# Optimization experiments

Hardware: AMD Instinct MI355X
Metric: run time of the kernel (lower is better)

The kernel has to match this reference:

```python
import jax, jax.numpy as jnp
import numpy as np

N, P, D = 262144, 128, 64
EPS = 1e-5
NEG = -1e30


def setup_inputs() -> dict:
    key = jax.random.key(0)
    ks = jax.random.split(key, 12)
    feature = jax.random.normal(ks[0], (N, D), jnp.float32)
    feature_geo = jax.random.normal(ks[1], (N, D), jnp.float32)
    xyz = jax.random.uniform(ks[2], (N, 3), jnp.float32)
    centers = jax.random.uniform(ks[3], (3,), jnp.float32)
    plane_center = jax.random.uniform(ks[4], (P, 3), jnp.float32)
    nrm = jax.random.normal(ks[5], (P, 3), jnp.float32)
    plane_normal = nrm / jnp.linalg.norm(nrm, axis=1, keepdims=True)
    lo = 0.3 * jax.random.uniform(ks[6], (P, 3), jnp.float32)
    hi = 0.5 + 0.5 * jax.random.uniform(ks[7], (P, 3), jnp.float32)
    # exactly two active axes per plane (one axis of the aabb is zeroed)
    ax = jnp.arange(P) % 3
    keep = (jnp.arange(3)[None, :] != ax[:, None]).astype(jnp.float32)
    plane_xyz_min = lo * keep
    plane_xyz_max = hi * keep
    w1 = 0.05 * jax.random.normal(ks[8], (2 * D, D), jnp.float32)
    b1 = jnp.zeros((D,), jnp.float32)
    w2 = 0.05 * jax.random.normal(ks[9], (D, D), jnp.float32)
    b2 = jnp.zeros((D,), jnp.float32)
    w3 = 0.05 * jax.random.normal(ks[10], (D, 1), jnp.float32)
    b3 = jnp.zeros((1,), jnp.float32)
    g1 = jnp.ones((D,), jnp.float32); be1 = jnp.zeros((D,), jnp.float32)
    m1 = jnp.zeros((D,), jnp.float32); v1 = jnp.ones((D,), jnp.float32)
    g2 = jnp.ones((D,), jnp.float32); be2 = jnp.zeros((D,), jnp.float32)
    m2 = jnp.zeros((D,), jnp.float32); v2 = jnp.ones((D,), jnp.float32)
    return dict(feature=feature, feature_geo=feature_geo, xyz=xyz, centers=centers,
                plane_center=plane_center, plane_normal=plane_normal,
                plane_xyz_min=plane_xyz_min, plane_xyz_max=plane_xyz_max,
                w1=w1, b1=b1, g1=g1, be1=be1, m1=m1, v1=v1,
                w2=w2, b2=b2, g2=g2, be2=be2, m2=m2, v2=v2,
                w3=w3, b3=b3)


def _bn(x, g, b, m, v):
    return (x - m) * (g * jax.lax.rsqrt(v + EPS)) + b


def reference(feature, feature_geo, xyz, centers, plane_center, plane_normal,
              plane_xyz_min, plane_xyz_max, w1, b1, g1, be1, m1, v1,
              w2, b2, g2, be2, m2, v2, w3, b3):
    clouds = xyz + centers                                   # [N,3]
    f = jnp.concatenate([feature, feature_geo], axis=1)      # [N,2D]
    # 1x1 conv MLP == per-point matmul (fc1 -> fc2 with BN+ReLU, fc3)
    h1 = jax.nn.relu(_bn(f @ w1 + b1, g1, be1, m1, v1))      # [N,D]
    h2 = jax.nn.relu(_bn(h1 @ w2 + b2, g2, be2, m2, v2))     # [N,D]
    scores = jax.nn.relu(h2 @ w3 + b3)[:, 0]                 # [N]
    # per-plane aabb mask over the two active axes (xyz_max != 0)
    active = plane_xyz_max != 0                              # [P,3]
    in_rng = (clouds[None] >= plane_xyz_min[:, None]) & (clouds[None] < plane_xyz_max[:, None])
    range_mask = jnp.all(in_rng | ~active[:, None, :], axis=-1)   # [P,N]
    # point-to-plane distance: |(clouds - center) . normal|
    dots = clouds @ plane_normal.T                           # [N,P]
    offs = jnp.sum(plane_center * plane_normal, axis=1)      # [P]
    dist = jnp.abs(dots - offs[None, :]).T                   # [P,N]
    mask = range_mask & (dist < 0.1)                         # [P,N]
    sig = jax.nn.sigmoid(scores)                             # [N]
    on_mask = mask & (sig > 0.5)[None, :]
    off_mask = mask & (sig <= 0.5)[None, :]

    def pool(m):  # masked max-pool of fc2 features over points of one plane
        val = jnp.max(jnp.where(m[:, None], h2, NEG), axis=0)     # [D]
        return jnp.where(jnp.any(m), val, 0.0)

    on_feat = jax.lax.map(pool, on_mask)                     # [P,D]
    off_feat = jax.lax.map(pool, off_mask)                   # [P,D]
    scores_masked = jnp.where(mask, scores[None, :], 0.0)    # [P,N]
    return scores_masked, mask, on_mask, off_mask, on_feat, off_feat
```

## Files before the change

kernel.cpp:

```cpp
#include <hip/hip_runtime.h>
#include <hip/hip_bf16.h>
#include <math.h>

#define NPTS 262144
#define NP   128
#define DD   64
#define NWORDS (NPTS / 64)

__global__ __launch_bounds__(256) void prep_kernel(
    const float* __restrict__ plane_center, const float* __restrict__ plane_normal,
    const float* __restrict__ pmin, const float* __restrict__ pmax,
    float* __restrict__ packed, float* __restrict__ out_feats)
{
    const int t = threadIdx.x;
    out_feats[blockIdx.x * 256 + t] = 0.0f;
    if (blockIdx.x == 0 && t < NP) {
        float n0 = plane_normal[t*3+0], n1 = plane_normal[t*3+1], n2 = plane_normal[t*3+2];
        float c0 = plane_center[t*3+0], c1 = plane_center[t*3+1], c2 = plane_center[t*3+2];
        float off = (c0*n0 + c1*n1) + c2*n2;
        float4* pp = reinterpret_cast<float4*>(packed) + t * 3;
        pp[0] = make_float4(n0, n1, n2, off);
        pp[1] = make_float4(pmin[t*3+0], pmin[t*3+1], pmin[t*3+2], 0.0f);
        pp[2] = make_float4(pmax[t*3+0], pmax[t*3+1], pmax[t*3+2], 0.0f);
    }
}

__global__ __launch_bounds__(256) void fused_kernel(
    const float* __restrict__ feature, const float* __restrict__ feature_geo,
    const float* __restrict__ xyz, const float* __restrict__ centers,
    const float* __restrict__ packed,
    const float* __restrict__ w1, const float* __restrict__ b1,
    const float* __restrict__ g1, const float* __restrict__ be1,
    const float* __restrict__ m1, const float* __restrict__ v1,
    const float* __restrict__ w2, const float* __restrict__ b2,
    const float* __restrict__ g2, const float* __restrict__ be2,
    const float* __restrict__ m2, const float* __restrict__ v2,
    const float* __restrict__ w3, const float* __restrict__ b3,
    float* __restrict__ h2_out,
    float* __restrict__ out_sm, float* __restrict__ out_mask,
    float* __restrict__ out_on, float* __restrict__ out_off,
    unsigned long long* __restrict__ hitOn, unsigned long long* __restrict__ hitOff)
{
    const int t = threadIdx.x;
    const int n = blockIdx.x * 256 + t;

    const float c0 = xyz[n*3+0] + centers[0];
    const float c1 = xyz[n*3+1] + centers[1];
    const float c2 = xyz[n*3+2] + centers[2];

    float acc[DD];
#pragma unroll
    for (int j = 0; j < DD; ++j) acc[j] = 0.0f;

    const float4* fA = reinterpret_cast<const float4*>(feature) + (size_t)n * 16;
#pragma unroll 1
    for (int q = 0; q < 16; ++q) {
        const float4 fv = fA[q];
        const float* wr = w1 + q * 4 * DD;
#pragma unroll
        for (int j = 0; j < DD; ++j) acc[j] = fmaf(fv.x, wr[j], acc[j]);
#pragma unroll
        for (int j = 0; j < DD; ++j) acc[j] = fmaf(fv.y, wr[DD + j], acc[j]);
#pragma unroll
        for (int j = 0; j < DD; ++j) acc[j] = fmaf(fv.z, wr[2 * DD + j], acc[j]);
#pragma unroll
        for (int j = 0; j < DD; ++j) acc[j] = fmaf(fv.w, wr[3 * DD + j], acc[j]);
    }
    const float4* fB = reinterpret_cast<const float4*>(feature_geo) + (size_t)n * 16;
    const float* w1b = w1 + DD * DD;
#pragma unroll 1
    for (int q = 0; q < 16; ++q) {
        const float4 fv = fB[q];
        const float* wr = w1b + q * 4 * DD;
#pragma unroll
        for (int j = 0; j < DD; ++j) acc[j] = fmaf(fv.x, wr[j], acc[j]);
#pragma unroll
        for (int j = 0; j < DD; ++j) acc[j] = fmaf(fv.y, wr[DD + j], acc[j]);
#pragma unroll
        for (int j = 0; j < DD; ++j) acc[j] = fmaf(fv.z, wr[2 * DD + j], acc[j]);
#pragma unroll
        for (int j = 0; j < DD; ++j) acc[j] = fmaf(fv.w, wr[3 * DD + j], acc[j]);
    }
    float h1[DD];
#pragma unroll
    for (int j = 0; j < DD; ++j) {
        float sc = g1[j] * (1.0f / sqrtf(v1[j] + 1e-5f));
        float h  = fmaf(acc[j] + b1[j] - m1[j], sc, be1[j]);
        h1[j] = fmaxf(h, 0.0f);
        acc[j] = 0.0f;
    }
#pragma unroll 1
    for (int q = 0; q < 16; ++q) {
        const float fx = h1[4*q+0], fy = h1[4*q+1], fz = h1[4*q+2], fw = h1[4*q+3];
        const float* wr = w2 + q * 4 * DD;
#pragma unroll
        for (int j = 0; j < DD; ++j) acc[j] = fmaf(fx, wr[j], acc[j]);
#pragma unroll
        for (int j = 0; j < DD; ++j) acc[j] = fmaf(fy, wr[DD + j], acc[j]);
#pragma unroll
        for (int j = 0; j < DD; ++j) acc[j] = fmaf(fz, wr[2 * DD + j], acc[j]);
#pragma unroll
        for (int j = 0; j < DD; ++j) acc[j] = fmaf(fw, wr[3 * DD + j], acc[j]);
    }
    float s = 0.0f;
#pragma unroll
    for (int j = 0; j < DD; ++j) {
        float sc = g2[j] * (1.0f / sqrtf(v2[j] + 1e-5f));
        float h  = fmaf(acc[j] + b2[j] - m2[j], sc, be2[j]);
        h = fmaxf(h, 0.0f);
        acc[j] = h;
        s = fmaf(h, w3[j], s);
    }
    s += b3[0];
    const float score = fmaxf(s, 0.0f);

    float4* o = reinterpret_cast<float4*>(h2_out) + (size_t)n * 16;
#pragma unroll
    for (int q = 0; q < 16; ++q)
        o[q] = make_float4(acc[4*q+0], acc[4*q+1], acc[4*q+2], acc[4*q+3]);

    const bool on  = (0.5f + 0.5f * tanhf(0.5f * score)) > 0.5f;
    const int lane = t & 63;
    const int word = n >> 6;

    const float4* pp = reinterpret_cast<const float4*>(packed);
#pragma unroll 1
    for (int p = 0; p < NP; ++p) {
        float4 nrm = pp[p*3+0];
        float4 mn  = pp[p*3+1];
        float4 mx  = pp[p*3+2];
        float d = fabsf(fmaf(c2, nrm.z, fmaf(c1, nrm.y, c0 * nrm.x)) - nrm.w);
        bool ok0 = (mx.x == 0.0f) | ((c0 >= mn.x) & (c0 < mx.x));
        bool ok1 = (mx.y == 0.0f) | ((c1 >= mn.y) & (c1 < mx.y));
        bool ok2 = (mx.z == 0.0f) | ((c2 >= mn.z) & (c2 < mx.z));
        bool mk  = ok0 & ok1 & ok2 & (d < 0.1f);
        size_t idx = (size_t)p * NPTS + n;
        out_sm[idx]   = mk ? score : 0.0f;
        out_mask[idx] = mk ? 1.0f : 0.0f;
        bool mon  = mk & on;
        bool moff = mk & (!on);
        out_on[idx]  = mon  ? 1.0f : 0.0f;
        out_off[idx] = moff ? 1.0f : 0.0f;
        unsigned long long bOn  = __ballot(mon);
        unsigned long long bOff = __ballot(moff);
        if (lane == 0) {
            hitOn [(size_t)p * NWORDS + word] = bOn;
            hitOff[(size_t)p * NWORDS + word] = bOff;
        }
    }
}

__global__ __launch_bounds__(256) void pool_kernel(
    const float* __restrict__ h2,
    const unsigned long long* __restrict__ hitOn,
    const unsigned long long* __restrict__ hitOff,
    int* __restrict__ out_feats_i)
{
    __shared__ float tile[128 * DD];
    __shared__ unsigned long long bm[2][NP][2];
    const int t = threadIdx.x;
    const int lane = t & 63;
    const int wv = t >> 6;

    float accOn[32], accOff[32];
#pragma unroll
    for (int i = 0; i < 32; ++i) { accOn[i] = 0.0f; accOff[i] = 0.0f; }

    for (int cc = 0; cc < 4; ++cc) {
        const int chunk = blockIdx.x * 4 + cc;
        const int base  = chunk * 128;
        const float4* src = reinterpret_cast<const float4*>(h2 + (size_t)base * DD);
        float4* dst = reinterpret_cast<float4*>(tile);
#pragma unroll
        for (int q = 0; q < 8; ++q) dst[t + q * 256] = src[t + q * 256];
        {
            const int p = t & 127;
            const int half = t >> 7;
            const unsigned long long* hsrc = half ? hitOff : hitOn;
            const int w0 = chunk * 2;
            bm[half][p][0] = hsrc[(size_t)p * NWORDS + w0 + 0];
            bm[half][p][1] = hsrc[(size_t)p * NWORDS + w0 + 1];
        }
        __syncthreads();

#pragma unroll
        for (int i = 0; i < 32; ++i) {
            const int p = wv * 32 + i;
            unsigned long long m;
            m = bm[0][p][0];
            while (m) { int nn = __builtin_ctzll(m); m &= m - 1;
                        accOn[i]  = fmaxf(accOn[i],  tile[nn * DD + lane]); }
            m = bm[0][p][1];
            while (m) { int nn = __builtin_ctzll(m); m &= m - 1;
                        accOn[i]  = fmaxf(accOn[i],  tile[(64 + nn) * DD + lane]); }
            m = bm[1][p][0];
            while (m) { int nn = __builtin_ctzll(m); m &= m - 1;
                        accOff[i] = fmaxf(accOff[i], tile[nn * DD + lane]); }
            m = bm[1][p][1];
            while (m) { int nn = __builtin_ctzll(m); m &= m - 1;
                        accOff[i] = fmaxf(accOff[i], tile[(64 + nn) * DD + lane]); }
        }
        __syncthreads();
    }
#pragma unroll
    for (int i = 0; i < 32; ++i) {
        const int p = wv * 32 + i;
        if (accOn[i]  != 0.0f) atomicMax(&out_feats_i[p * DD + lane],            __float_as_int(accOn[i]));
        if (accOff[i] != 0.0f) atomicMax(&out_feats_i[NP * DD + p * DD + lane],  __float_as_int(accOff[i]));
    }
}

extern "C" void kernel_launch(void* const* d_in, const int* in_sizes, int n_in,
                              void* d_out, int out_size, void* d_ws, size_t ws_size,
                              hipStream_t stream) {
    const float* feature      = (const float*)d_in[0];
    const float* feature_geo  = (const float*)d_in[1];
    const float* xyz          = (const float*)d_in[2];
    const float* centers      = (const float*)d_in[3];
    const float* plane_center = (const float*)d_in[4];
    const float* plane_normal = (const float*)d_in[5];
    const float* pmin         = (const float*)d_in[6];
    const float* pmax         = (const float*)d_in[7];
    const float* w1 = (const float*)d_in[8];
    const float* b1 = (const float*)d_in[9];
    const float* g1 = (const float*)d_in[10];
    const float* be1 = (const float*)d_in[11];
    const float* m1 = (const float*)d_in[12];
    const float* v1 = (const float*)d_in[13];
    const float* w2 = (const float*)d_in[14];
    const float* b2 = (const float*)d_in[15];
    const float* g2 = (const float*)d_in[16];
    const float* be2 = (const float*)d_in[17];
    const float* m2 = (const float*)d_in[18];
    const float* v2 = (const float*)d_in[19];
    const float* w3 = (const float*)d_in[20];
    const float* b3 = (const float*)d_in[21];

    float* out = (float*)d_out;
    const size_t PN = (size_t)NP * NPTS;
    float* out_sm    = out;
    float* out_mask  = out + PN;
    float* out_on    = out + 2 * PN;
    float* out_off   = out + 3 * PN;
    float* out_feats = out + 4 * PN;

    float* h2     = (float*)d_ws;
    unsigned long long* hitOn  = (unsigned long long*)(h2 + (size_t)NPTS * DD);
    unsigned long long* hitOff = hitOn + (size_t)NP * NWORDS;
    float* packed = (float*)(hitOff + (size_t)NP * NWORDS);

    prep_kernel<<<64, 256, 0, stream>>>(
        plane_center, plane_normal, pmin, pmax, packed, out_feats);
    fused_kernel<<<NPTS / 256, 256, 0, stream>>>(
        feature, feature_geo, xyz, centers, packed,
        w1, b1, g1, be1, m1, v1, w2, b2, g2, be2, m2, v2, w3, b3,
        h2, out_sm, out_mask, out_on, out_off, hitOn, hitOff);
    pool_kernel<<<512, 256, 0, stream>>>(h2, hitOn, hitOff, (int*)out_feats);
}
```

Measured before the change: 842.5 us.

## Cut fused kernel register pressure, prefetch loads, use nontemporal mask stores

The fused kernel now asks for 4 blocks per SM through launch_bounds. The second layer is computed in two halves of 32 outputs so only 32 accumulators are live at once, with h2 written out per half. Feature loads and the per-plane parameters are software-prefetched one iteration ahead. The large mask outputs are written with nontemporal stores to bypass cache pollution. The occupancy bound could force register spills, and splitting layer 2 reads the h1 values twice.

```diff
diff --git a/kernel.cpp b/kernel.cpp
--- a/kernel.cpp
+++ b/kernel.cpp
@@ -25,7 +25,7 @@
     }
 }
 
-__global__ __launch_bounds__(256) void fused_kernel(
+__global__ __launch_bounds__(256, 4) void fused_kernel(
     const float* __restrict__ feature, const float* __restrict__ feature_geo,
     const float* __restrict__ xyz, const float* __restrict__ centers,
     const float* __restrict__ packed,
@@ -53,9 +53,12 @@
     for (int j = 0; j < DD; ++j) acc[j] = 0.0f;
 
     const float4* fA = reinterpret_cast<const float4*>(feature) + (size_t)n * 16;
+    const float4* fB = reinterpret_cast<const float4*>(feature_geo) + (size_t)n * 16;
+    float4 nxt = fA[0];
 #pragma unroll 1
     for (int q = 0; q < 16; ++q) {
-        const float4 fv = fA[q];
+        const float4 fv = nxt;
+        nxt = fA[(q + 1) & 15];
         const float* wr = w1 + q * 4 * DD;
 #pragma unroll
         for (int j = 0; j < DD; ++j) acc[j] = fmaf(fv.x, wr[j], acc[j]);
@@ -66,11 +69,12 @@
 #pragma unroll
         for (int j = 0; j < DD; ++j) acc[j] = fmaf(fv.w, wr[3 * DD + j], acc[j]);
     }
-    const float4* fB = reinterpret_cast<const float4*>(feature_geo) + (size_t)n * 16;
     const float* w1b = w1 + DD * DD;
+    nxt = fB[0];
 #pragma unroll 1
     for (int q = 0; q < 16; ++q) {
-        const float4 fv = fB[q];
+        const float4 fv = nxt;
+        nxt = fB[(q + 1) & 15];
         const float* wr = w1b + q * 4 * DD;
 #pragma unroll
         for (int j = 0; j < DD; ++j) acc[j] = fmaf(fv.x, wr[j], acc[j]);
@@ -87,66 +91,76 @@
         float sc = g1[j] * (1.0f / sqrtf(v1[j] + 1e-5f));
         float h  = fmaf(acc[j] + b1[j] - m1[j], sc, be1[j]);
         h1[j] = fmaxf(h, 0.0f);
-        acc[j] = 0.0f;
-    }
-#pragma unroll 1
-    for (int q = 0; q < 16; ++q) {
-        const float fx = h1[4*q+0], fy = h1[4*q+1], fz = h1[4*q+2], fw = h1[4*q+3];
-        const float* wr = w2 + q * 4 * DD;
-#pragma unroll
-        for (int j = 0; j < DD; ++j) acc[j] = fmaf(fx, wr[j], acc[j]);
-#pragma unroll
-        for (int j = 0; j < DD; ++j) acc[j] = fmaf(fy, wr[DD + j], acc[j]);
-#pragma unroll
-        for (int j = 0; j < DD; ++j) acc[j] = fmaf(fz, wr[2 * DD + j], acc[j]);
-#pragma unroll
-        for (int j = 0; j < DD; ++j) acc[j] = fmaf(fw, wr[3 * DD + j], acc[j]);
-    }
+    }
+
     float s = 0.0f;
-#pragma unroll
-    for (int j = 0; j < DD; ++j) {
-        float sc = g2[j] * (1.0f / sqrtf(v2[j] + 1e-5f));
-        float h  = fmaf(acc[j] + b2[j] - m2[j], sc, be2[j]);
-        h = fmaxf(h, 0.0f);
-        acc[j] = h;
-        s = fmaf(h, w3[j], s);
+    float4* o = reinterpret_cast<float4*>(h2_out) + (size_t)n * 16;
+#pragma unroll 1
+    for (int hh = 0; hh < 2; ++hh) {
+        float a2[32];
+#pragma unroll
+        for (int j = 0; j < 32; ++j) a2[j] = 0.0f;
+        const float* w2h = w2 + hh * 32;
+#pragma unroll 1
+        for (int q = 0; q < 16; ++q) {
+            const float fx = h1[4*q+0], fy = h1[4*q+1], fz = h1[4*q+2], fw = h1[4*q+3];
+            const float* wr = w2h + q * 4 * DD;
+#pragma unroll
+            for (int j = 0; j < 32; ++j) a2[j] = fmaf(fx, wr[j], a2[j]);
+#pragma unroll
+            for (int j = 0; j < 32; ++j) a2[j] = fmaf(fy, wr[DD + j], a2[j]);
+#pragma unroll
+            for (int j = 0; j < 32; ++j) a2[j] = fmaf(fz, wr[2 * DD + j], a2[j]);
+#pragma unroll
+            for (int j = 0; j < 32; ++j) a2[j] = fmaf(fw, wr[3 * DD + j], a2[j]);
+        }
+#pragma unroll
+        for (int j = 0; j < 32; ++j) {
+            const int jj = hh * 32 + j;
+            float sc = g2[jj] * (1.0f / sqrtf(v2[jj] + 1e-5f));
+            float h  = fmaf(a2[j] + b2[jj] - m2[jj], sc, be2[jj]);
+            h = fmaxf(h, 0.0f);
+            a2[j] = h;
+            s = fmaf(h, w3[jj], s);
+        }
+#pragma unroll
+        for (int q = 0; q < 8; ++q)
+            o[hh * 8 + q] = make_float4(a2[4*q+0], a2[4*q+1], a2[4*q+2], a2[4*q+3]);
     }
     s += b3[0];
     const float score = fmaxf(s, 0.0f);
-
-    float4* o = reinterpret_cast<float4*>(h2_out) + (size_t)n * 16;
-#pragma unroll
-    for (int q = 0; q < 16; ++q)
-        o[q] = make_float4(acc[4*q+0], acc[4*q+1], acc[4*q+2], acc[4*q+3]);
 
     const bool on  = (0.5f + 0.5f * tanhf(0.5f * score)) > 0.5f;
     const int lane = t & 63;
     const int word = n >> 6;
 
     const float4* pp = reinterpret_cast<const float4*>(packed);
+    float4 nrm = pp[0], mn = pp[1], mx = pp[2];
 #pragma unroll 1
     for (int p = 0; p < NP; ++p) {
-        float4 nrm = pp[p*3+0];
-        float4 mn  = pp[p*3+1];
-        float4 mx  = pp[p*3+2];
+        const int pn = ((p + 1) & 127) * 3;
+        float4 nrmN = pp[pn + 0];
+        float4 mnN  = pp[pn + 1];
+        float4 mxN  = pp[pn + 2];
         float d = fabsf(fmaf(c2, nrm.z, fmaf(c1, nrm.y, c0 * nrm.x)) - nrm.w);
         bool ok0 = (mx.x == 0.0f) | ((c0 >= mn.x) & (c0 < mx.x));
         bool ok1 = (mx.y == 0.0f) | ((c1 >= mn.y) & (c1 < mx.y));
         bool ok2 = (mx.z == 0.0f) | ((c2 >= mn.z) & (c2 < mx.z));
         bool mk  = ok0 & ok1 & ok2 & (d < 0.1f);
         size_t idx = (size_t)p * NPTS + n;
-        out_sm[idx]   = mk ? score : 0.0f;
-        out_mask[idx] = mk ? 1.0f : 0.0f;
         bool mon  = mk & on;
         bool moff = mk & (!on);
-        out_on[idx]  = mon  ? 1.0f : 0.0f;
-        out_off[idx] = moff ? 1.0f : 0.0f;
+        __builtin_nontemporal_store(mk ? score : 0.0f, &out_sm[idx]);
+        __builtin_nontemporal_store(mk ? 1.0f : 0.0f,  &out_mask[idx]);
+        __builtin_nontemporal_store(mon ? 1.0f : 0.0f, &out_on[idx]);
+        __builtin_nontemporal_store(moff ? 1.0f : 0.0f,&out_off[idx]);
         unsigned long long bOn  = __ballot(mon);
         unsigned long long bOff = __ballot(moff);
         if (lane == 0) {
             hitOn [(size_t)p * NWORDS + word] = bOn;
             hitOff[(size_t)p * NWORDS + word] = bOff;
         }
+        nrm = nrmN; mn = mnN; mx = mxN;
     }
 }
 
```

Result: no change. 851.8 us (+1.1%).
